# Optimization experiments

Measured on AMD Instinct MI355X. Metric: run time of the kernel, lower is better.

## Reference

```python
import jax, jax.numpy as jnp
import numpy as np

N, C, H_IMG, W_IMG = 32, 3, 224, 224
P = 14                      # number_patches per side
PH, PW = H_IMG // P, W_IMG // P
IN_DIM = C * PH * PW        # 768
D = 768                     # hidden_dimension
NH = 12                     # number_heads
DH = D // NH                # 64
L = 12                      # number_blocks
OUT = 1000                  # output_dimension
S = P * P + 1               # 197 tokens (cls + patches)
MLP = 4 * D                 # mlp_ratio * d


def sinusoidal_pos_emb(s, d):
    # result[i][j] = sin(i / 10000^(j/d)) if j even else cos(i / 10000^((j-1)/d))
    i = np.arange(s, dtype=np.float64)[:, None]
    j = np.arange(d)[None, :]
    angle = i / (10000.0 ** ((j - (j % 2)) / float(d)))
    emb = np.where(j % 2 == 0, np.sin(angle), np.cos(angle))
    return jnp.asarray(emb, jnp.float32)


def setup_inputs() -> dict:
    key = jax.random.key(0)
    ks = jax.random.split(key, 12)
    f32 = jnp.float32
    p = {}
    p['images'] = jax.random.normal(ks[0], (N, C, H_IMG, W_IMG), f32)
    p['W_map'] = jax.random.normal(ks[1], (IN_DIM, D), f32) * 0.02
    p['b_map'] = jnp.zeros((D,), f32)
    p['class_token'] = jax.random.normal(ks[2], (1, D), f32)
    p['pos_emb'] = sinusoidal_pos_emb(S, D)  # frozen (requires_grad=False)
    p['ln1_g'] = jnp.ones((L, D), f32)
    p['ln1_b'] = jnp.zeros((L, D), f32)
    p['Wq'] = jax.random.normal(ks[3], (L, NH, DH, DH), f32) * 0.02
    p['bq'] = jnp.zeros((L, NH, DH), f32)
    p['Wk'] = jax.random.normal(ks[4], (L, NH, DH, DH), f32) * 0.02
    p['bk'] = jnp.zeros((L, NH, DH), f32)
    p['Wv'] = jax.random.normal(ks[5], (L, NH, DH, DH), f32) * 0.02
    p['bv'] = jnp.zeros((L, NH, DH), f32)
    p['ln2_g'] = jnp.ones((L, D), f32)
    p['ln2_b'] = jnp.zeros((L, D), f32)
    p['W1'] = jax.random.normal(ks[6], (L, D, MLP), f32) * 0.02
    p['b1'] = jnp.zeros((L, MLP), f32)
    p['W2'] = jax.random.normal(ks[7], (L, MLP, D), f32) * 0.02
    p['b2'] = jnp.zeros((L, D), f32)
    p['W_head'] = jax.random.normal(ks[8], (D, OUT), f32) * 0.02
    p['b_head'] = jnp.zeros((OUT,), f32)
    return p


def _layer_norm(x, g, b, eps=1e-5):
    mu = jnp.mean(x, axis=-1, keepdims=True)
    var = jnp.var(x, axis=-1, keepdims=True)
    return (x - mu) * jax.lax.rsqrt(var + eps) * g + b


def reference(images, W_map, b_map, class_token, pos_emb, ln1_g, ln1_b,
              Wq, bq, Wk, bk, Wv, bv, ln2_g, ln2_b, W1, b1, W2, b2,
              W_head, b_head):
    n = images.shape[0]
    # patchify: [N,C,H,W] -> [N, P*P, C*ph*pw]; per-patch flatten is (C,ph,pw) order
    patches = images.reshape(n, C, P, PH, P, PW)
    patches = patches.transpose(0, 2, 4, 1, 3, 5).reshape(n, P * P, IN_DIM)
    tokens = patches @ W_map + b_map                         # [N, P*P, D]
    cls = jnp.broadcast_to(class_token[None], (n, 1, D))
    x = jnp.concatenate([cls, tokens], axis=1) + pos_emb     # [N, S, D]

    scale = DH ** 0.5
    for l in range(L):
        # --- MHSA with per-head independent Linear weights ---
        h = _layer_norm(x, ln1_g[l], ln1_b[l])
        xh = h.reshape(n, S, NH, DH)
        q = jnp.einsum('nshd,hde->nshe', xh, Wq[l]) + bq[l]
        k = jnp.einsum('nshd,hde->nshe', xh, Wk[l]) + bk[l]
        v = jnp.einsum('nshd,hde->nshe', xh, Wv[l]) + bv[l]
        scores = jnp.einsum('nqhd,nkhd->nhqk', q, k) / scale  # [N,H,S,S]
        attn = jax.nn.softmax(scores, axis=-1)
        o = jnp.einsum('nhqk,nkhd->nqhd', attn, v).reshape(n, S, D)
        x = x + o
        # --- MLP (exact GELU, as torch.nn.GELU default) ---
        h2 = _layer_norm(x, ln2_g[l], ln2_b[l])
        m = jax.nn.gelu(h2 @ W1[l] + b1[l], approximate=False) @ W2[l] + b2[l]
        x = x + m

    logits = x[:, 0] @ W_head + b_head
    return jax.nn.softmax(logits, axis=-1)
```

## Files before the change

### kernel.cpp

```cpp
#include <hip/hip_runtime.h>
#include <hip/hip_bf16.h>

constexpr int N_   = 32;
constexpr int C_   = 3;
constexpr int P_   = 14;
constexpr int PHW  = 16;
constexpr int IND  = 768;
constexpr int D_   = 768;
constexpr int NH_  = 12;
constexpr int DH_  = 64;
constexpr int L_   = 12;
constexpr int OUT_ = 1000;
constexpr int S_   = 197;
constexpr int MLP_ = 3072;
constexpr int NPATCH = P_ * P_;
constexpr int ROWS   = N_ * S_;
constexpr int TROWS  = N_ * NPATCH;
constexpr int RPAD   = 6400;
constexpr int SP_R   = 256;
constexpr int SP_C   = 224;

typedef __attribute__((ext_vector_type(8))) short bf16x8;
typedef __attribute__((ext_vector_type(4))) float f32x4;

__device__ __forceinline__ float bf2f(ushort u) {
    union { float f; unsigned int i; } v; v.i = ((unsigned int)u) << 16; return v.f;
}
__device__ __forceinline__ ushort f2bf(float f) {
    union { float f; unsigned int i; } v; v.f = f;
    unsigned int r = v.i + 0x7fffu + ((v.i >> 16) & 1u);
    return (ushort)(r >> 16);
}

__global__ __launch_bounds__(256)
void mfma_gemm(const ushort* __restrict__ Ag,
               const ushort* __restrict__ Bg,
               void* __restrict__ Cg,
               const float* __restrict__ biasg,
               int M, int N, int K,
               int lda, int ldb, int ldc,
               long offA1, long offA2,
               long offB1, long offB2,
               long offC1, long offC2,
               long offS1, long offS2,
               int inner, float alpha, int act, int outbf, int accum)
{
    const int bz = blockIdx.z;
    const int bi = bz / inner, bj = bz % inner;
    const ushort* A = Ag + bi * offA1 + bj * offA2;
    const ushort* B = Bg + bi * offB1 + bj * offB2;
    const long coff = bi * offC1 + bj * offC2;
    const float* bias = biasg ? (biasg + bi * offS1 + bj * offS2) : nullptr;

    __shared__ ushort As[128 * 32];
    __shared__ ushort Bs[128 * 32];

    const int tid  = threadIdx.x;
    const int w    = tid >> 6;
    const int lhi  = (tid & 63) >> 4;
    const int llo  = tid & 15;
    const int wr   = w >> 1, wc = w & 1;
    const int row0 = blockIdx.y * 128;
    const int col0 = blockIdx.x * 128;

    f32x4 acc[4][4];
#pragma unroll
    for (int m = 0; m < 4; ++m)
#pragma unroll
        for (int n = 0; n < 4; ++n) acc[m][n] = (f32x4){0.f, 0.f, 0.f, 0.f};

    int r0s = (0 * 256 + tid) >> 2, s0s = tid & 3;
    int r1s = (1 * 256 + tid) >> 2, s1s = tid & 3;
    int ss0 = s0s ^ ((r0s >> 1) & 3);
    int ss1 = s1s ^ ((r1s >> 1) & 3);
    ushort* dstA0 = As + ((0 * 256 + (w << 6)) << 3);
    ushort* dstA1 = As + ((1 * 256 + (w << 6)) << 3);
    ushort* dstB0 = Bs + ((0 * 256 + (w << 6)) << 3);
    ushort* dstB1 = Bs + ((1 * 256 + (w << 6)) << 3);

    for (int k0 = 0; k0 < K; k0 += 32) {
        const ushort* a0 = A + (long)(row0 + r0s) * lda + k0 + ss0 * 8;
        const ushort* a1 = A + (long)(row0 + r1s) * lda + k0 + ss1 * 8;
        const ushort* b0 = B + (long)(col0 + r0s) * ldb + k0 + ss0 * 8;
        const ushort* b1 = B + (long)(col0 + r1s) * ldb + k0 + ss1 * 8;
        __builtin_amdgcn_global_load_lds((const __attribute__((address_space(1))) void*)a0,
                                         (__attribute__((address_space(3))) void*)dstA0, 16, 0, 0);
        __builtin_amdgcn_global_load_lds((const __attribute__((address_space(1))) void*)a1,
                                         (__attribute__((address_space(3))) void*)dstA1, 16, 0, 0);
        __builtin_amdgcn_global_load_lds((const __attribute__((address_space(1))) void*)b0,
                                         (__attribute__((address_space(3))) void*)dstB0, 16, 0, 0);
        __builtin_amdgcn_global_load_lds((const __attribute__((address_space(1))) void*)b1,
                                         (__attribute__((address_space(3))) void*)dstB1, 16, 0, 0);
        __syncthreads();

        bf16x8 av[4], bv[4];
#pragma unroll
        for (int m = 0; m < 4; ++m) {
            int R = wr * 64 + m * 16 + llo;
            av[m] = *(const bf16x8*)(As + R * 32 + ((lhi ^ ((R >> 1) & 3)) << 3));
        }
#pragma unroll
        for (int n = 0; n < 4; ++n) {
            int R = wc * 64 + n * 16 + llo;
            bv[n] = *(const bf16x8*)(Bs + R * 32 + ((lhi ^ ((R >> 1) & 3)) << 3));
        }
#pragma unroll
        for (int m = 0; m < 4; ++m)
#pragma unroll
            for (int n = 0; n < 4; ++n)
                acc[m][n] = __builtin_amdgcn_mfma_f32_16x16x32_bf16(av[m], bv[n], acc[m][n], 0, 0, 0);
        __syncthreads();
    }

    float* Cf = (float*)Cg + coff;
    ushort* Ch = (ushort*)Cg + coff;
#pragma unroll
    for (int m = 0; m < 4; ++m) {
#pragma unroll
        for (int n = 0; n < 4; ++n) {
#pragma unroll
            for (int j = 0; j < 4; ++j) {
                int gr = row0 + wr * 64 + m * 16 + lhi * 4 + j;
                int gc = col0 + wc * 64 + n * 16 + llo;
                if (gr < M && gc < N) {
                    float v = acc[m][n][j] * alpha;
                    if (bias) v += bias[gc];
                    if (act == 1) v = 0.5f * v * (1.f + erff(v * 0.70710678118654752f));
                    long ci = (long)gr * ldc + gc;
                    if (outbf) {
                        Ch[ci] = f2bf(v);
                    } else {
                        if (accum) v += Cf[ci];
                        Cf[ci] = v;
                    }
                }
            }
        }
    }
}

__global__ __launch_bounds__(256)
void im2col_kernel(const float* __restrict__ img, ushort* __restrict__ patches)
{
    long idx = (long)blockIdx.x * 256 + threadIdx.x;
    if (idx >= (long)TROWS * IND) return;
    int e = (int)(idx % IND);
    int t = (int)((idx / IND) % NPATCH);
    int n = (int)(idx / ((long)IND * NPATCH));
    int pw = e & 15, ph = (e >> 4) & 15, c = e >> 8;
    int px = t % P_, py = t / P_;
    patches[idx] = f2bf(img[(((long)n * C_ + c) * 224 + py * PHW + ph) * 224 + px * PHW + pw]);
}

__global__ __launch_bounds__(256)
void assemble_kernel(const float* __restrict__ tokens,
                     const float* __restrict__ cls,
                     const float* __restrict__ pos,
                     float* __restrict__ x)
{
    long idx = (long)blockIdx.x * 256 + threadIdx.x;
    if (idx >= (long)ROWS * D_) return;
    int d = (int)(idx % D_);
    int s = (int)((idx / D_) % S_);
    long n = idx / ((long)D_ * S_);
    float v = (s == 0) ? cls[d] : tokens[((long)n * NPATCH + (s - 1)) * D_ + d];
    x[idx] = v + pos[(long)s * D_ + d];
}

__global__ __launch_bounds__(256)
void layernorm_kernel(const float* __restrict__ x, ushort* __restrict__ out,
                      const float* __restrict__ g, const float* __restrict__ b)
{
    long row = blockIdx.x;
    const float* xr = x + row * D_;
    ushort* orow = out + row * D_;
    int tid = threadIdx.x;
    float v0 = xr[tid], v1 = xr[tid + 256], v2 = xr[tid + 512];
    float s  = v0 + v1 + v2;
    float sq = v0 * v0 + v1 * v1 + v2 * v2;
    for (int off = 32; off > 0; off >>= 1) {
        s  += __shfl_down(s, off);
        sq += __shfl_down(sq, off);
    }
    __shared__ float rs[4], rq[4];
    int wave = tid >> 6, lane = tid & 63;
    if (lane == 0) { rs[wave] = s; rq[wave] = sq; }
    __syncthreads();
    float S  = rs[0] + rs[1] + rs[2] + rs[3];
    float SQ = rq[0] + rq[1] + rq[2] + rq[3];
    float mean = S * (1.f / 768.f);
    float var  = SQ * (1.f / 768.f) - mean * mean;
    float rstd = rsqrtf(var + 1e-5f);
    orow[tid]       = f2bf((v0 - mean) * rstd * g[tid]       + b[tid]);
    orow[tid + 256] = f2bf((v1 - mean) * rstd * g[tid + 256] + b[tid + 256]);
    orow[tid + 512] = f2bf((v2 - mean) * rstd * g[tid + 512] + b[tid + 512]);
}

__global__ __launch_bounds__(256)
void softmax197_kernel(ushort* __restrict__ scores)
{
    long rid = (long)blockIdx.x * 4 + (threadIdx.x >> 6);
    if (rid >= (long)N_ * NH_ * S_) return;
    long batch = rid / S_;
    long r = rid % S_;
    ushort* p = scores + (batch * SP_R + r) * SP_C;
    int lane = threadIdx.x & 63;
    float v[4];
    float mx = -INFINITY;
#pragma unroll
    for (int i = 0; i < 4; ++i) {
        int idx = lane + i * 64;
        v[i] = (idx < S_) ? bf2f(p[idx]) : -INFINITY;
        mx = fmaxf(mx, v[i]);
    }
    for (int off = 32; off > 0; off >>= 1) mx = fmaxf(mx, __shfl_xor(mx, off));
    float sum = 0.f;
#pragma unroll
    for (int i = 0; i < 4; ++i) {
        int idx = lane + i * 64;
        if (idx < S_) { v[i] = expf(v[i] - mx); sum += v[i]; }
    }
    for (int off = 32; off > 0; off >>= 1) sum += __shfl_xor(sum, off);
    float inv = 1.f / sum;
#pragma unroll
    for (int i = 0; i < 4; ++i) {
        int idx = lane + i * 64;
        if (idx < SP_C) p[idx] = (idx < S_) ? f2bf(v[i] * inv) : (ushort)0;
    }
}

__global__ __launch_bounds__(256)
void vtrans_kernel(const ushort* __restrict__ qkv, ushort* __restrict__ Vt)
{
    int b = blockIdx.z;
    int n = b / NH_, h = b % NH_;
    __shared__ ushort t[32][33];
    int s0 = blockIdx.x * 32, d0 = blockIdx.y * 32;
    int tx = threadIdx.x & 31, ty = threadIdx.x >> 5;
#pragma unroll
    for (int i = 0; i < 4; ++i) {
        int s = s0 + ty * 4 + i;
        ushort v = 0;
        if (s < S_) v = qkv[(long)(n * S_ + s) * 2304 + 1536 + h * 64 + d0 + tx];
        t[ty * 4 + i][tx] = v;
    }
    __syncthreads();
#pragma unroll
    for (int i = 0; i < 4; ++i) {
        int dh = d0 + ty * 4 + i;
        int s  = s0 + tx;
        Vt[((long)b * 64 + dh) * SP_C + s] = t[tx][ty * 4 + i];
    }
}

__global__ __launch_bounds__(256)
void transcast_kernel(const float* __restrict__ in, ushort* __restrict__ out,
                      int R, int C, long inL, long outL)
{
    const float* ip = in + (long)blockIdx.z * inL;
    ushort* op = out + (long)blockIdx.z * outL;
    __shared__ float t[32][33];
    int c0 = blockIdx.x * 32, r0 = blockIdx.y * 32;
    int tx = threadIdx.x & 31, ty = threadIdx.x >> 5;
#pragma unroll
    for (int i = 0; i < 4; ++i) {
        int r = r0 + ty * 4 + i, c = c0 + tx;
        float v = 0.f;
        if (r < R && c < C) v = ip[(long)r * C + c];
        t[ty * 4 + i][tx] = v;
    }
    __syncthreads();
#pragma unroll
    for (int i = 0; i < 4; ++i) {
        int c = c0 + ty * 4 + i, r = r0 + tx;
        if (c < C && r < R) op[(long)c * R + r] = f2bf(t[tx][ty * 4 + i]);
    }
}

__global__ __launch_bounds__(256)
void transf32_kernel(const float* __restrict__ in, float* __restrict__ out, int R, int C)
{
    __shared__ float t[32][33];
    int c0 = blockIdx.x * 32, r0 = blockIdx.y * 32;
    int tx = threadIdx.x & 31, ty = threadIdx.x >> 5;
#pragma unroll
    for (int i = 0; i < 4; ++i) {
        int r = r0 + ty * 4 + i, c = c0 + tx;
        float v = 0.f;
        if (r < R && c < C) v = in[(long)r * C + c];
        t[ty * 4 + i][tx] = v;
    }
    __syncthreads();
#pragma unroll
    for (int i = 0; i < 4; ++i) {
        int c = c0 + ty * 4 + i, r = r0 + tx;
        if (c < C && r < R) out[(long)c * R + r] = t[tx][ty * 4 + i];
    }
}

__global__ __launch_bounds__(256)
void build_wqkvC_kernel(const float* __restrict__ Wq, const float* __restrict__ Wk,
                        const float* __restrict__ Wv, int l0, ushort* __restrict__ out)
{
    long idx = (long)blockIdx.x * 256 + threadIdx.x;
    if (idx >= 36L * 4096) return;
    int z = blockIdx.z, l = l0 + z;
    int sec = (int)(idx / 49152);
    int r   = (int)(idx % 49152);
    int h = r / 4096, rr = r % 4096, e = rr / 64, d = rr % 64;
    const float* W = sec == 0 ? Wq : (sec == 1 ? Wk : Wv);
    out[(long)z * 147456 + idx] = f2bf(W[(((long)l * NH_ + h) * 64 + d) * 64 + e]);
}

__global__ __launch_bounds__(256)
void build_bqkv_kernel(const float* __restrict__ bq, const float* __restrict__ bk,
                       const float* __restrict__ bv, float* __restrict__ out)
{
    int i = blockIdx.x * 256 + threadIdx.x;
    if (i >= L_ * 2304) return;
    int l = i / 2304, n = i % 2304;
    int sec = n / 768, h = (n % 768) / 64, e = n % 64;
    const float* b = sec == 0 ? bq : (sec == 1 ? bk : bv);
    out[i] = b[((long)l * NH_ + h) * 64 + e];
}

__global__ __launch_bounds__(256)
void head_kernel(const float* __restrict__ x, const float* __restrict__ Wt,
                 const float* __restrict__ bhead, float* __restrict__ logits)
{
    int wid = blockIdx.x * 4 + (threadIdx.x >> 6);
    int lane = threadIdx.x & 63;
    int n = wid / OUT_, c = wid % OUT_;
    if (n >= N_) return;
    const float* xr = x + (long)n * S_ * D_;
    const float* wr = Wt + (long)c * D_;
    float acc = 0.f;
#pragma unroll
    for (int i = 0; i < 12; ++i) acc += xr[lane + i * 64] * wr[lane + i * 64];
    for (int off = 32; off > 0; off >>= 1) acc += __shfl_down(acc, off);
    if (lane == 0) logits[(long)n * OUT_ + c] = acc + bhead[c];
}

__global__ __launch_bounds__(256)
void softmax_out_kernel(const float* __restrict__ logits, float* __restrict__ out)
{
    int row = blockIdx.x;
    int tid = threadIdx.x;
    const float* p = logits + (long)row * OUT_;
    float v[4];
    float mx = -INFINITY;
#pragma unroll
    for (int i = 0; i < 4; ++i) {
        int idx = tid + i * 256;
        v[i] = (idx < OUT_) ? p[idx] : -INFINITY;
        mx = fmaxf(mx, v[i]);
    }
    int wave = tid >> 6, lane = tid & 63;
    for (int off = 32; off > 0; off >>= 1) mx = fmaxf(mx, __shfl_xor(mx, off));
    __shared__ float r1[4], r2[4];
    if (lane == 0) r1[wave] = mx;
    __syncthreads();
    mx = fmaxf(fmaxf(r1[0], r1[1]), fmaxf(r1[2], r1[3]));
    float sum = 0.f;
#pragma unroll
    for (int i = 0; i < 4; ++i) {
        int idx = tid + i * 256;
        if (idx < OUT_) { v[i] = expf(v[i] - mx); sum += v[i]; }
    }
    for (int off = 32; off > 0; off >>= 1) sum += __shfl_xor(sum, off);
    if (lane == 0) r2[wave] = sum;
    __syncthreads();
    sum = r2[0] + r2[1] + r2[2] + r2[3];
    float inv = 1.f / sum;
#pragma unroll
    for (int i = 0; i < 4; ++i) {
        int idx = tid + i * 256;
        if (idx < OUT_) out[(long)row * OUT_ + idx] = v[i] * inv;
    }
}

extern "C" void kernel_launch(void* const* d_in, const int* in_sizes, int n_in,
                              void* d_out, int out_size, void* d_ws, size_t ws_size,
                              hipStream_t stream)
{
    const float* images = (const float*)d_in[0];
    const float* W_map  = (const float*)d_in[1];
    const float* b_map  = (const float*)d_in[2];
    const float* cls    = (const float*)d_in[3];
    const float* pos    = (const float*)d_in[4];
    const float* ln1_g  = (const float*)d_in[5];
    const float* ln1_b  = (const float*)d_in[6];
    const float* Wq     = (const float*)d_in[7];
    const float* bq     = (const float*)d_in[8];
    const float* Wk     = (const float*)d_in[9];
    const float* bk     = (const float*)d_in[10];
    const float* Wv     = (const float*)d_in[11];
    const float* bv     = (const float*)d_in[12];
    const float* ln2_g  = (const float*)d_in[13];
    const float* ln2_b  = (const float*)d_in[14];
    const float* W1     = (const float*)d_in[15];
    const float* b1     = (const float*)d_in[16];
    const float* W2     = (const float*)d_in[17];
    const float* b2     = (const float*)d_in[18];
    const float* W_head = (const float*)d_in[19];
    const float* b_head = (const float*)d_in[20];

    char* base = (char*)d_ws;
    float*  x       = (float*)base;   base += 19660800L;
    ushort* hbuf    = (ushort*)base;  base += 9830400L;
    ushort* qkv     = (ushort*)base;  base += 29491200L;
    ushort* Vt      = (ushort*)base;  base += 11038720L;
    ushort* scoresP = (ushort*)base;  base += 44040192L;
    ushort* mbuf    = (ushort*)base;  base += 39321600L;
    ushort* Wmapt   = (ushort*)base;  base += 1179648L;
    float*  bqkvA   = (float*)base;   base += 110592L;
    ushort* WqkvC   = (ushort*)base;  base += 3538944L;

    size_t used = (size_t)(base - (char*)d_ws);
    const long W1L_ALL = 56623104L, W2L_ALL = 56623104L;
    const long W1L_ONE = 4718592L,  W2L_ONE = 4718592L;
    bool hoist = ws_size >= used + (size_t)(W1L_ALL + W2L_ALL);
    ushort* W1tA = (ushort*)base;  base += hoist ? W1L_ALL : W1L_ONE;
    ushort* W2tA = (ushort*)base;  base += hoist ? W2L_ALL : W2L_ONE;
    const long w1str = hoist ? 3072L * 768 : 0;
    const long w2str = hoist ? 768L * 3072 : 0;

    float* W_headT = (float*)scoresP;
    float* logits  = (float*)((char*)scoresP + 3072000L);
    float*  tokens  = (float*)scoresP;
    ushort* patches = mbuf;

    build_wqkvC_kernel<<<dim3(576, 1, L_), 256, 0, stream>>>(Wq, Wk, Wv, 0, WqkvC);
    build_bqkv_kernel<<<(L_ * 2304 + 255) / 256, 256, 0, stream>>>(bq, bk, bv, bqkvA);
    transcast_kernel<<<dim3(24, 24, 1), 256, 0, stream>>>(W_map, Wmapt, IND, D_, 0L, 0L);
    if (hoist) {
        transcast_kernel<<<dim3(96, 24, L_), 256, 0, stream>>>(W1, W1tA, D_, MLP_,
                                                               (long)D_ * MLP_, 3072L * 768);
        transcast_kernel<<<dim3(24, 96, L_), 256, 0, stream>>>(W2, W2tA, MLP_, D_,
                                                               (long)MLP_ * D_, 768L * 3072);
    }

    {
        long tot = (long)TROWS * IND;
        im2col_kernel<<<(int)((tot + 255) / 256), 256, 0, stream>>>(images, patches);
    }
    mfma_gemm<<<dim3(D_ / 128, TROWS / 128, 1), 256, 0, stream>>>(
        patches, Wmapt, tokens, b_map,
        TROWS, D_, IND, IND, IND, D_,
        0L, 0L, 0L, 0L, 0L, 0L, 0L, 0L, 1, 1.f, 0, 0, 0);
    {
        long tot = (long)ROWS * D_;
        assemble_kernel<<<(int)((tot + 255) / 256), 256, 0, stream>>>(tokens, cls, pos, x);
    }

    for (int l = 0; l < L_; ++l) {
        layernorm_kernel<<<ROWS, 256, 0, stream>>>(x, hbuf, ln1_g + (long)l * D_, ln1_b + (long)l * D_);

        mfma_gemm<<<dim3(1, RPAD / 128, 36), 256, 0, stream>>>(
            hbuf, WqkvC + (long)l * 147456, qkv, bqkvA + (long)l * 2304,
            ROWS, 64, 64, D_, 64, 2304,
            0L, 64L,
            12L * 4096, 4096L,
            768L, 64L,
            768L, 64L,
            12, 1.f, 0, 1, 0);

        vtrans_kernel<<<dim3(7, 2, N_ * NH_), 256, 0, stream>>>(qkv, Vt);

        mfma_gemm<<<dim3(2, 2, N_ * NH_), 256, 0, stream>>>(
            qkv, qkv + 768, scoresP, nullptr,
            S_, S_, DH_, 2304, 2304, SP_C,
            (long)S_ * 2304, 64L, (long)S_ * 2304, 64L,
            (long)NH_ * SP_R * SP_C, (long)SP_R * SP_C, 0L, 0L,
            NH_, 0.125f, 0, 1, 0);

        softmax197_kernel<<<(N_ * NH_ * S_ + 3) / 4, 256, 0, stream>>>(scoresP);

        mfma_gemm<<<dim3(1, 2, N_ * NH_), 256, 0, stream>>>(
            scoresP, Vt, x, nullptr,
            S_, DH_, SP_C, SP_C, SP_C, D_,
            (long)NH_ * SP_R * SP_C, (long)SP_R * SP_C,
            (long)NH_ * 64 * SP_C, (long)64 * SP_C,
            (long)S_ * D_, 64L, 0L, 0L,
            NH_, 1.f, 0, 0, 1);

        layernorm_kernel<<<ROWS, 256, 0, stream>>>(x, hbuf, ln2_g + (long)l * D_, ln2_b + (long)l * D_);

        if (!hoist)
            transcast_kernel<<<dim3(96, 24, 1), 256, 0, stream>>>(
                W1 + (long)l * D_ * MLP_, W1tA, D_, MLP_, 0L, 0L);
        mfma_gemm<<<dim3(MLP_ / 128, RPAD / 128, 1), 256, 0, stream>>>(
            hbuf, W1tA + (long)l * w1str, mbuf, b1 + (long)l * MLP_,
            ROWS, MLP_, D_, D_, D_, MLP_,
            0L, 0L, 0L, 0L, 0L, 0L, 0L, 0L, 1, 1.f, 1, 1, 0);

        if (!hoist)
            transcast_kernel<<<dim3(24, 96, 1), 256, 0, stream>>>(
                W2 + (long)l * MLP_ * D_, W2tA, MLP_, D_, 0L, 0L);
        mfma_gemm<<<dim3(D_ / 128, RPAD / 128, 1), 256, 0, stream>>>(
            mbuf, W2tA + (long)l * w2str, x, b2 + (long)l * D_,
            ROWS, D_, MLP_, MLP_, MLP_, D_,
            0L, 0L, 0L, 0L, 0L, 0L, 0L, 0L, 1, 1.f, 0, 0, 1);
    }

    transf32_kernel<<<dim3(32, 24), 256, 0, stream>>>(W_head, W_headT, D_, OUT_);
    head_kernel<<<(N_ * OUT_) / 4, 256, 0, stream>>>(x, W_headT, b_head, logits);
    softmax_out_kernel<<<N_, 256, 0, stream>>>(logits, (float*)d_out);
}
```

Before: 4.472 ms.

## Double-buffer GEMM LDS tiles, add XCD-aware block swizzle, fuse V transpose

The GEMM kernel now double-buffers its LDS tiles. It issues the next K-tile's global-to-LDS loads before computing the current tile and uses explicit vmcnt waits and barriers, so memory latency can overlap with MFMA work. Large dense GEMMs also get a workgroup remapping, so blocks dispatched round-robin across the eight XCDs work on neighbouring tiles and share L2. The QKV GEMM writes V directly in transposed layout, which removes the separate vtrans kernel launch each layer. The costs are twice the LDS use, which may reduce occupancy, and scattered 2-byte stores in the V epilogue.

```diff
diff --git a/kernel.cpp b/kernel.cpp
--- a/kernel.cpp
+++ b/kernel.cpp
@@ -43,7 +43,8 @@
                long offB1, long offB2,
                long offC1, long offC2,
                long offS1, long offS2,
-               int inner, float alpha, int act, int outbf, int accum)
+               int inner, float alpha, int act, int outbf, int accum,
+               int swz, ushort* __restrict__ vtout)
 {
     const int bz = blockIdx.z;
     const int bi = bz / inner, bj = bz % inner;
@@ -52,16 +53,28 @@
     const long coff = bi * offC1 + bj * offC2;
     const float* bias = biasg ? (biasg + bi * offS1 + bj * offS2) : nullptr;
 
-    __shared__ ushort As[128 * 32];
-    __shared__ ushort Bs[128 * 32];
+    int bx = blockIdx.x, by = blockIdx.y;
+    if (swz) {
+        const int gx = gridDim.x;
+        const int nwg = gx * gridDim.y;
+        const int orig = by * gx + bx;
+        const int q = nwg >> 3, r = nwg & 7;
+        const int xcd = orig & 7, loc = orig >> 3;
+        const int wgid = (xcd < r ? xcd * (q + 1) : r * (q + 1) + (xcd - r) * q) + loc;
+        bx = wgid % gx;
+        by = wgid / gx;
+    }
+
+    __shared__ ushort As[2][128 * 32];
+    __shared__ ushort Bs[2][128 * 32];
 
     const int tid  = threadIdx.x;
     const int w    = tid >> 6;
     const int lhi  = (tid & 63) >> 4;
     const int llo  = tid & 15;
     const int wr   = w >> 1, wc = w & 1;
-    const int row0 = blockIdx.y * 128;
-    const int col0 = blockIdx.x * 128;
+    const int row0 = by * 128;
+    const int col0 = bx * 128;
 
     f32x4 acc[4][4];
 #pragma unroll
@@ -69,51 +82,72 @@
 #pragma unroll
         for (int n = 0; n < 4; ++n) acc[m][n] = (f32x4){0.f, 0.f, 0.f, 0.f};
 
-    int r0s = (0 * 256 + tid) >> 2, s0s = tid & 3;
-    int r1s = (1 * 256 + tid) >> 2, s1s = tid & 3;
-    int ss0 = s0s ^ ((r0s >> 1) & 3);
-    int ss1 = s1s ^ ((r1s >> 1) & 3);
-    ushort* dstA0 = As + ((0 * 256 + (w << 6)) << 3);
-    ushort* dstA1 = As + ((1 * 256 + (w << 6)) << 3);
-    ushort* dstB0 = Bs + ((0 * 256 + (w << 6)) << 3);
-    ushort* dstB1 = Bs + ((1 * 256 + (w << 6)) << 3);
-
-    for (int k0 = 0; k0 < K; k0 += 32) {
-        const ushort* a0 = A + (long)(row0 + r0s) * lda + k0 + ss0 * 8;
-        const ushort* a1 = A + (long)(row0 + r1s) * lda + k0 + ss1 * 8;
-        const ushort* b0 = B + (long)(col0 + r0s) * ldb + k0 + ss0 * 8;
-        const ushort* b1 = B + (long)(col0 + r1s) * ldb + k0 + ss1 * 8;
-        __builtin_amdgcn_global_load_lds((const __attribute__((address_space(1))) void*)a0,
-                                         (__attribute__((address_space(3))) void*)dstA0, 16, 0, 0);
-        __builtin_amdgcn_global_load_lds((const __attribute__((address_space(1))) void*)a1,
-                                         (__attribute__((address_space(3))) void*)dstA1, 16, 0, 0);
-        __builtin_amdgcn_global_load_lds((const __attribute__((address_space(1))) void*)b0,
-                                         (__attribute__((address_space(3))) void*)dstB0, 16, 0, 0);
-        __builtin_amdgcn_global_load_lds((const __attribute__((address_space(1))) void*)b1,
-                                         (__attribute__((address_space(3))) void*)dstB1, 16, 0, 0);
-        __syncthreads();
+    const int r0s = tid >> 2,        s0s = tid & 3;
+    const int r1s = 64 + (tid >> 2), s1s = tid & 3;
+    const int ss0 = s0s ^ ((r0s >> 1) & 3);
+    const int ss1 = s1s ^ ((r1s >> 1) & 3);
+    const int dst0 = (w << 6) << 3;
+    const int dst1 = (256 + (w << 6)) << 3;
+
+    const long arow0 = (long)(row0 + r0s) * lda + ss0 * 8;
+    const long arow1 = (long)(row0 + r1s) * lda + ss1 * 8;
+    const long brow0 = (long)(col0 + r0s) * ldb + ss0 * 8;
+    const long brow1 = (long)(col0 + r1s) * ldb + ss1 * 8;
+
+#define STAGE(buf, k0)                                                                     \
+    do {                                                                                   \
+        __builtin_amdgcn_global_load_lds(                                                  \
+            (const __attribute__((address_space(1))) void*)(A + arow0 + (k0)),             \
+            (__attribute__((address_space(3))) void*)(&As[buf][0] + dst0), 16, 0, 0);      \
+        __builtin_amdgcn_global_load_lds(                                                  \
+            (const __attribute__((address_space(1))) void*)(A + arow1 + (k0)),             \
+            (__attribute__((address_space(3))) void*)(&As[buf][0] + dst1), 16, 0, 0);      \
+        __builtin_amdgcn_global_load_lds(                                                  \
+            (const __attribute__((address_space(1))) void*)(B + brow0 + (k0)),             \
+            (__attribute__((address_space(3))) void*)(&Bs[buf][0] + dst0), 16, 0, 0);      \
+        __builtin_amdgcn_global_load_lds(                                                  \
+            (const __attribute__((address_space(1))) void*)(B + brow1 + (k0)),             \
+            (__attribute__((address_space(3))) void*)(&Bs[buf][0] + dst1), 16, 0, 0);      \
+    } while (0)
+
+    const int nt = K >> 5;
+    STAGE(0, 0);
+    for (int t = 0; t < nt; ++t) {
+        const int cur = t & 1;
+        if (t + 1 < nt) {
+            STAGE(cur ^ 1, (t + 1) << 5);
+            asm volatile("s_waitcnt vmcnt(4)" ::: "memory");
+        } else {
+            asm volatile("s_waitcnt vmcnt(0)" ::: "memory");
+        }
+        __builtin_amdgcn_s_barrier();
+        asm volatile("" ::: "memory");
 
         bf16x8 av[4], bv[4];
 #pragma unroll
         for (int m = 0; m < 4; ++m) {
             int R = wr * 64 + m * 16 + llo;
-            av[m] = *(const bf16x8*)(As + R * 32 + ((lhi ^ ((R >> 1) & 3)) << 3));
+            av[m] = *(const bf16x8*)(&As[cur][0] + R * 32 + ((lhi ^ ((R >> 1) & 3)) << 3));
         }
 #pragma unroll
         for (int n = 0; n < 4; ++n) {
             int R = wc * 64 + n * 16 + llo;
-            bv[n] = *(const bf16x8*)(Bs + R * 32 + ((lhi ^ ((R >> 1) & 3)) << 3));
+            bv[n] = *(const bf16x8*)(&Bs[cur][0] + R * 32 + ((lhi ^ ((R >> 1) & 3)) << 3));
         }
 #pragma unroll
         for (int m = 0; m < 4; ++m)
 #pragma unroll
             for (int n = 0; n < 4; ++n)
                 acc[m][n] = __builtin_amdgcn_mfma_f32_16x16x32_bf16(av[m], bv[n], acc[m][n], 0, 0, 0);
-        __syncthreads();
-    }
+
+        asm volatile("" ::: "memory");
+        __builtin_amdgcn_s_barrier();
+    }
+#undef STAGE
 
     float* Cf = (float*)Cg + coff;
     ushort* Ch = (ushort*)Cg + coff;
+    const bool vpath = (vtout != nullptr) && (bi == 2);
 #pragma unroll
     for (int m = 0; m < 4; ++m) {
 #pragma unroll
@@ -122,10 +156,14 @@
             for (int j = 0; j < 4; ++j) {
                 int gr = row0 + wr * 64 + m * 16 + lhi * 4 + j;
                 int gc = col0 + wc * 64 + n * 16 + llo;
-                if (gr < M && gc < N) {
-                    float v = acc[m][n][j] * alpha;
-                    if (bias) v += bias[gc];
-                    if (act == 1) v = 0.5f * v * (1.f + erff(v * 0.70710678118654752f));
+                if (gr >= M || gc >= N) continue;
+                float v = acc[m][n][j] * alpha;
+                if (bias) v += bias[gc];
+                if (act == 1) v = 0.5f * v * (1.f + erff(v * 0.70710678118654752f));
+                if (vpath) {
+                    int nn = gr / 197, s = gr - nn * 197;
+                    vtout[(((long)nn * NH_ + bj) * 64 + gc) * SP_C + s] = f2bf(v);
+                } else {
                     long ci = (long)gr * ldc + gc;
                     if (outbf) {
                         Ch[ci] = f2bf(v);
@@ -226,30 +264,6 @@
     for (int i = 0; i < 4; ++i) {
         int idx = lane + i * 64;
         if (idx < SP_C) p[idx] = (idx < S_) ? f2bf(v[i] * inv) : (ushort)0;
-    }
-}
-
-__global__ __launch_bounds__(256)
-void vtrans_kernel(const ushort* __restrict__ qkv, ushort* __restrict__ Vt)
-{
-    int b = blockIdx.z;
-    int n = b / NH_, h = b % NH_;
-    __shared__ ushort t[32][33];
-    int s0 = blockIdx.x * 32, d0 = blockIdx.y * 32;
-    int tx = threadIdx.x & 31, ty = threadIdx.x >> 5;
-#pragma unroll
-    for (int i = 0; i < 4; ++i) {
-        int s = s0 + ty * 4 + i;
-        ushort v = 0;
-        if (s < S_) v = qkv[(long)(n * S_ + s) * 2304 + 1536 + h * 64 + d0 + tx];
-        t[ty * 4 + i][tx] = v;
-    }
-    __syncthreads();
-#pragma unroll
-    for (int i = 0; i < 4; ++i) {
-        int dh = d0 + ty * 4 + i;
-        int s  = s0 + tx;
-        Vt[((long)b * 64 + dh) * SP_C + s] = t[tx][ty * 4 + i];
     }
 }
 
@@ -447,7 +461,7 @@
     mfma_gemm<<<dim3(D_ / 128, TROWS / 128, 1), 256, 0, stream>>>(
         patches, Wmapt, tokens, b_map,
         TROWS, D_, IND, IND, IND, D_,
-        0L, 0L, 0L, 0L, 0L, 0L, 0L, 0L, 1, 1.f, 0, 0, 0);
+        0L, 0L, 0L, 0L, 0L, 0L, 0L, 0L, 1, 1.f, 0, 0, 0, 1, nullptr);
     {
         long tot = (long)ROWS * D_;
         assemble_kernel<<<(int)((tot + 255) / 256), 256, 0, stream>>>(tokens, cls, pos, x);
@@ -463,16 +477,14 @@
             12L * 4096, 4096L,
             768L, 64L,
             768L, 64L,
-            12, 1.f, 0, 1, 0);
-
-        vtrans_kernel<<<dim3(7, 2, N_ * NH_), 256, 0, stream>>>(qkv, Vt);
+            12, 1.f, 0, 1, 0, 0, Vt);
 
         mfma_gemm<<<dim3(2, 2, N_ * NH_), 256, 0, stream>>>(
             qkv, qkv + 768, scoresP, nullptr,
             S_, S_, DH_, 2304, 2304, SP_C,
             (long)S_ * 2304, 64L, (long)S_ * 2304, 64L,
             (long)NH_ * SP_R * SP_C, (long)SP_R * SP_C, 0L, 0L,
-            NH_, 0.125f, 0, 1, 0);
+            NH_, 0.125f, 0, 1, 0, 0, nullptr);
 
         softmax197_kernel<<<(N_ * NH_ * S_ + 3) / 4, 256, 0, stream>>>(scoresP);
 
@@ -482,7 +494,7 @@
             (long)NH_ * SP_R * SP_C, (long)SP_R * SP_C,
             (long)NH_ * 64 * SP_C, (long)64 * SP_C,
             (long)S_ * D_, 64L, 0L, 0L,
-            NH_, 1.f, 0, 0, 1);
+            NH_, 1.f, 0, 0, 1, 0, nullptr);
 
         layernorm_kernel<<<ROWS, 256, 0, stream>>>(x, hbuf, ln2_g + (long)l * D_, ln2_b + (long)l * D_);
 
@@ -492,7 +504,7 @@
         mfma_gemm<<<dim3(MLP_ / 128, RPAD / 128, 1), 256, 0, stream>>>(
             hbuf, W1tA + (long)l * w1str, mbuf, b1 + (long)l * MLP_,
             ROWS, MLP_, D_, D_, D_, MLP_,
-            0L, 0L, 0L, 0L, 0L, 0L, 0L, 0L, 1, 1.f, 1, 1, 0);
+            0L, 0L, 0L, 0L, 0L, 0L, 0L, 0L, 1, 1.f, 1, 1, 0, 1, nullptr);
 
         if (!hoist)
             transcast_kernel<<<dim3(24, 96, 1), 256, 0, stream>>>(
@@ -500,7 +512,7 @@
         mfma_gemm<<<dim3(D_ / 128, RPAD / 128, 1), 256, 0, stream>>>(
             mbuf, W2tA + (long)l * w2str, x, b2 + (long)l * D_,
             ROWS, D_, MLP_, MLP_, MLP_, D_,
-            0L, 0L, 0L, 0L, 0L, 0L, 0L, 0L, 1, 1.f, 0, 0, 1);
+            0L, 0L, 0L, 0L, 0L, 0L, 0L, 0L, 1, 1.f, 0, 0, 1, 1, nullptr);
     }
 
     transf32_kernel<<<dim3(32, 24), 256, 0, stream>>>(W_head, W_headT, D_, OUT_);
```

Measured after the change: 4.305 ms. 1.04x faster.
